# Performance work log

Hardware: AMD Instinct MI355X
Metric: run time of the kernel (lower is better)

Reference implementation:

```python
import jax, jax.numpy as jnp
import numpy as np


def setup_inputs() -> dict:
    key = jax.random.key(0)
    k1, k2, k3 = jax.random.split(key, 3)
    B, C, H, W = 32, 2048, 14, 14
    OUT = 512
    x = jax.random.normal(k1, (B, C, H, W), dtype=jnp.float32)
    gamma = jnp.zeros((1,), dtype=jnp.float32)  # nn.Parameter(torch.zeros(1))
    # 1x1 conv 2048 -> 512 (layer=4 branch), kaiming-ish scale
    conv_w = jax.random.normal(k2, (OUT, C, 1, 1), dtype=jnp.float32) * (1.0 / np.sqrt(C))
    conv_b = jax.random.normal(k3, (OUT,), dtype=jnp.float32) * 0.01
    return {"x": x, "gamma": gamma, "conv_w": conv_w, "conv_b": conv_b}


def reference(x, gamma, conv_w, conv_b):
    B, C, H, W = x.shape
    q = x.reshape(B, C, H * W)                      # [B, C, N]
    # energy[b, c, d] = <q[b,c,:], q[b,d,:]>
    energy = jnp.einsum('bcn,bdn->bcd', q, q)       # [B, C, C]
    # max-subtract trick: softmax(max - energy) along last dim
    energy_new = jnp.max(energy, axis=-1, keepdims=True) - energy
    attention = jax.nn.softmax(energy_new, axis=-1)  # [B, C, C]
    out = jnp.einsum('bcd,bdn->bcn', attention, q).reshape(B, C, H, W)
    out = gamma * out + x
    # 1x1 conv, stride 1, no padding (layer=4 branch)
    pam_out = jax.lax.conv_general_dilated(
        out, conv_w, window_strides=(1, 1), padding='VALID',
        dimension_numbers=('NCHW', 'OIHW', 'NCHW'))
    pam_out = pam_out + conv_b[None, :, None, None]
    return pam_out
```

## Files before the change

### kernel.cpp

```cpp
#include <hip/hip_runtime.h>
#include <hip/hip_bf16.h>
#include <stdint.h>

#define B_   32
#define C_   2048
#define HW_  196
#define OUT_ 512
#define KT_  128
#define MT_  64
#define NKT  (C_ / KT_)

typedef short short8 __attribute__((ext_vector_type(8)));
typedef float floatx4 __attribute__((ext_vector_type(4)));
typedef unsigned short u16;

#define VMCNT_WAIT(n) __builtin_amdgcn_s_waitcnt(0x0F70 | (n))

__device__ __forceinline__ uint32_t pack_bf16(float a, float b) {
  union { __hip_bfloat162 h; uint32_t u; } c;
  c.h = __float22bfloat162_rn(make_float2(a, b));
  return c.u;
}

__device__ __forceinline__ void async_ld16(const u16* g, void* lds_base) {
  __builtin_amdgcn_global_load_lds(
      (const __attribute__((address_space(1))) uint32_t*)g,
      (__attribute__((address_space(3))) uint32_t*)lds_base, 16, 0, 0);
}

__global__ void wcvt_kernel(const float* __restrict__ w, u16* __restrict__ wbf) {
  int gid = blockIdx.x * 256 + threadIdx.x;
  float4 v = ((const float4*)w)[gid];
  ((uint2*)wbf)[gid] = make_uint2(pack_bf16(v.x, v.y), pack_bf16(v.z, v.w));
}

__global__ void attn_fallback(const float* __restrict__ x, const float* __restrict__ gamma,
                              float* __restrict__ y) {
  float g = gamma[0];
  if (g == 0.0f) return;
  __shared__ float qc[HW_];
  __shared__ float e[C_];
  __shared__ float red[256];
  int tid = threadIdx.x;
  for (int cRow = blockIdx.x; cRow < C_; cRow += gridDim.x) {
    for (int b = 0; b < B_; ++b) {
      const float* q = x + (size_t)b * C_ * HW_;
      __syncthreads();
      for (int i = tid; i < HW_; i += 256) qc[i] = q[(size_t)cRow * HW_ + i];
      __syncthreads();
      for (int d = tid; d < C_; d += 256) {
        float s = 0.f;
        const float* qd = q + (size_t)d * HW_;
        for (int n = 0; n < HW_; ++n) s += qc[n] * qd[n];
        e[d] = s;
      }
      __syncthreads();
      float mn = 3.4e38f;
      for (int d = tid; d < C_; d += 256) mn = fminf(mn, e[d]);
      red[tid] = mn; __syncthreads();
      for (int s = 128; s > 0; s >>= 1) { if (tid < s) red[tid] = fminf(red[tid], red[tid + s]); __syncthreads(); }
      float emin = red[0];
      __syncthreads();
      float ps = 0.f;
      for (int d = tid; d < C_; d += 256) { float p = __expf(emin - e[d]); e[d] = p; ps += p; }
      red[tid] = ps; __syncthreads();
      for (int s = 128; s > 0; s >>= 1) { if (tid < s) red[tid] += red[tid + s]; __syncthreads(); }
      float S = red[0];
      __syncthreads();
      float invS = 1.f / S;
      for (int n = tid; n < HW_; n += 256) {
        float acc = 0.f;
        for (int d = 0; d < C_; ++d) acc += e[d] * q[(size_t)d * HW_ + n];
        y[((size_t)b * C_ + cRow) * HW_ + n] = g * acc * invS + q[(size_t)cRow * HW_ + n];
      }
    }
  }
}

__global__ __launch_bounds__(256, 3) void xpose_kernel(
    const float* __restrict__ x, const float* __restrict__ ysrc,
    const float* __restrict__ gamma, u16* __restrict__ xT) {
  __shared__ float tile[64 * 197];
  const float* src = (gamma[0] != 0.f) ? ysrc : x;
  int b  = blockIdx.x >> 5;
  int c0 = (blockIdx.x & 31) * 64;
  const float* sb = src + ((size_t)b * C_ + c0) * HW_;
  int tid = threadIdx.x;
  for (int r = 0; r < 13; ++r) {
    int u = r * 256 + tid;
    if (u < 3136) {
      int ci = u / 49, n4 = u - ci * 49;
      float4 v = *(const float4*)(sb + (size_t)ci * HW_ + n4 * 4);
      float* tp = &tile[ci * 197 + n4 * 4];
      tp[0] = v.x; tp[1] = v.y; tp[2] = v.z; tp[3] = v.w;
    }
  }
  __syncthreads();
  u16* xTb = xT + (size_t)b * HW_ * C_ + c0;
  for (int r = 0; r < 7; ++r) {
    int u = r * 256 + tid;
    if (u < 1568) {
      int c8 = u & 7, n = u >> 3;
      const float* tp = &tile[c8 * 8 * 197 + n];
      uint4 o;
      o.x = pack_bf16(tp[0 * 197], tp[1 * 197]);
      o.y = pack_bf16(tp[2 * 197], tp[3 * 197]);
      o.z = pack_bf16(tp[4 * 197], tp[5 * 197]);
      o.w = pack_bf16(tp[6 * 197], tp[7 * 197]);
      *(uint4*)(xTb + (size_t)n * C_ + c8 * 8) = o;
    }
  }
}

template<int P>
__device__ __forceinline__ void gemm_body(
    const u16* __restrict__ xT, const u16* __restrict__ wbf,
    const float* __restrict__ bias, float* __restrict__ out,
    u16* lds0, u16* lds1, int b, int oBase, int n0) {

  int tid  = threadIdx.x;
  int wave = tid >> 6;
  int lane = tid & 63;
  int col  = lane & 15;
  int quad = lane >> 4;

  const u16* xTb  = xT + (size_t)b * HW_ * C_;
  const u16* aPtr = wbf + (size_t)(oBase + wave * 16 + col) * C_;
  int maxRel = HW_ - 1 - n0;

  floatx4 acc[P];
#pragma unroll
  for (int i = 0; i < P; ++i) { floatx4 z = {0.f, 0.f, 0.f, 0.f}; acc[i] = z; }

  const u16* bPtr[P];
  int ldsOff[P];
#pragma unroll
  for (int jj = 0; jj < P; ++jj) {
    int n    = 4 * wave + quad + 16 * jj;
    int srcN = n0 + (n > maxRel ? maxRel : n);
    int kc   = col ^ (n & 7);
    bPtr[jj]   = xTb + (size_t)srcN * C_ + kc * 8;
    ldsOff[jj] = (wave + 4 * jj) * 512;
  }

  int aK = 0;
  auto issueB = [&](u16* dst) {
#pragma unroll
    for (int jj = 0; jj < P; ++jj) {
      async_ld16(bPtr[jj], dst + ldsOff[jj]);
      bPtr[jj] += KT_;
    }
  };
  uint4 aR[4];
  auto loadA = [&]() {
#pragma unroll
    for (int ks = 0; ks < 4; ++ks)
      aR[ks] = *(const uint4*)(aPtr + aK + ks * 32 + quad * 8);
    aK += KT_;
  };
  auto phase = [&](const u16* buf) {
#pragma unroll
    for (int ks = 0; ks < 4; ++ks) {
      union { uint4 u; short8 v; } af; af.u = aR[ks];
      int chunk = (ks * 4 + quad) ^ (col & 7);
      const u16* base = buf + col * KT_ + chunk * 8;
#pragma unroll
      for (int nt = 0; nt < P; ++nt) {
        short8 bf = *(const short8*)(base + nt * 16 * KT_);
        acc[nt] = __builtin_amdgcn_mfma_f32_16x16x32_bf16(af.v, bf, acc[nt], 0, 0, 0);
      }
    }
  };

  issueB(lds0);
  loadA();
  issueB(lds1);
  u16* cur = lds0; u16* nxt = lds1;
#pragma unroll
  for (int kt = 0; kt < NKT - 1; ++kt) {
    VMCNT_WAIT(P);
    __builtin_amdgcn_s_barrier();
    phase(cur);
    loadA();
    __builtin_amdgcn_s_barrier();
    if (kt < NKT - 2) issueB(cur);
    u16* t = cur; cur = nxt; nxt = t;
  }
  VMCNT_WAIT(0);
  __builtin_amdgcn_s_barrier();
  phase(cur);

  int nLim = HW_ - n0; if (nLim > 16 * P) nLim = 16 * P;
  float* outb = out + (size_t)b * OUT_ * HW_;
#pragma unroll
  for (int r = 0; r < 4; ++r) {
    int o = oBase + wave * 16 + quad * 4 + r;
    float bv = bias[o];
    float* orow = outb + (size_t)o * HW_ + n0;
#pragma unroll
    for (int nt = 0; nt < P; ++nt) {
      int nl = nt * 16 + col;
      if (nl < nLim) orow[nl] = acc[nt][r] + bv;
    }
  }
}

__global__ __launch_bounds__(256, 2) void conv_gemm(
    const u16* __restrict__ xT, const u16* __restrict__ wbf,
    const float* __restrict__ bias, float* __restrict__ out) {

  __shared__ __align__(16) u16 Bs2[2][112 * KT_];

  int bid = blockIdx.x;
  int xcd = bid & 7;
  int s   = bid >> 3;
  int ot  = s & 7;
  int g   = ((s >> 3) << 3) | xcd;
  int b   = g >> 1;
  int nh  = g & 1;

  if (nh == 0)
    gemm_body<7>(xT, wbf, bias, out, Bs2[0], Bs2[1], b, ot * MT_, 0);
  else
    gemm_body<6>(xT, wbf, bias, out, Bs2[0], Bs2[1], b, ot * MT_, 112);
}

extern "C" void kernel_launch(void* const* d_in, const int* in_sizes, int n_in,
                              void* d_out, int out_size, void* d_ws, size_t ws_size,
                              hipStream_t stream) {
  const float* x      = (const float*)d_in[0];
  const float* gamma  = (const float*)d_in[1];
  const float* conv_w = (const float*)d_in[2];
  const float* conv_b = (const float*)d_in[3];
  float* out = (float*)d_out;

  const size_t wbf_bytes = (size_t)OUT_ * C_ * sizeof(u16);
  const size_t xT_bytes  = (size_t)B_ * HW_ * C_ * sizeof(u16);
  const size_t y_bytes   = (size_t)B_ * C_ * HW_ * sizeof(float);
  u16*   wbf = (u16*)d_ws;
  u16*   xT  = (u16*)((char*)d_ws + wbf_bytes);
  float* yws = (float*)((char*)d_ws + wbf_bytes + xT_bytes);
  bool have_fallback_ws = ws_size >= wbf_bytes + xT_bytes + y_bytes;
  const float* ysrc = have_fallback_ws ? (const float*)yws : x;

  wcvt_kernel<<<dim3((OUT_ * C_) / 4 / 256), dim3(256), 0, stream>>>(conv_w, wbf);
  if (have_fallback_ws)
    attn_fallback<<<dim3(256), dim3(256), 0, stream>>>(x, gamma, yws);
  xpose_kernel<<<dim3(B_ * 32), dim3(256), 0, stream>>>(x, ysrc, gamma, xT);
  conv_gemm<<<dim3(512), dim3(256), 0, stream>>>(xT, wbf, conv_b, out);
}
```

Measured before the change: 127.1 us.

## Fuse transpose into GEMM staging and merge weight-convert with attention kernel

```diff
diff --git a/kernel.cpp b/kernel.cpp
--- a/kernel.cpp
+++ b/kernel.cpp
@@ -7,14 +7,13 @@
 #define HW_  196
 #define OUT_ 512
 #define KT_  128
-#define MT_  64
 #define NKT  (C_ / KT_)
+#define BN_  112
+#define LDSS 132
 
 typedef short short8 __attribute__((ext_vector_type(8)));
 typedef float floatx4 __attribute__((ext_vector_type(4)));
 typedef unsigned short u16;
-
-#define VMCNT_WAIT(n) __builtin_amdgcn_s_waitcnt(0x0F70 | (n))
 
 __device__ __forceinline__ uint32_t pack_bf16(float a, float b) {
   union { __hip_bfloat162 h; uint32_t u; } c;
@@ -22,27 +21,25 @@
   return c.u;
 }
 
-__device__ __forceinline__ void async_ld16(const u16* g, void* lds_base) {
-  __builtin_amdgcn_global_load_lds(
-      (const __attribute__((address_space(1))) uint32_t*)g,
-      (__attribute__((address_space(3))) uint32_t*)lds_base, 16, 0, 0);
-}
-
-__global__ void wcvt_kernel(const float* __restrict__ w, u16* __restrict__ wbf) {
-  int gid = blockIdx.x * 256 + threadIdx.x;
-  float4 v = ((const float4*)w)[gid];
-  ((uint2*)wbf)[gid] = make_uint2(pack_bf16(v.x, v.y), pack_bf16(v.z, v.w));
-}
-
-__global__ void attn_fallback(const float* __restrict__ x, const float* __restrict__ gamma,
-                              float* __restrict__ y) {
-  float g = gamma[0];
-  if (g == 0.0f) return;
+#define BAR_SYNC() asm volatile("s_waitcnt lgkmcnt(0)\n\ts_barrier" ::: "memory")
+
+__global__ void prep_kernel(const float* __restrict__ w, u16* __restrict__ wbf,
+                            const float* __restrict__ x,
+                            const float* __restrict__ gamma,
+                            float* __restrict__ y) {
+  if (blockIdx.x < 1024) {
+    int gid = blockIdx.x * 256 + threadIdx.x;
+    float4 v = ((const float4*)w)[gid];
+    ((uint2*)wbf)[gid] = make_uint2(pack_bf16(v.x, v.y), pack_bf16(v.z, v.w));
+    return;
+  }
+  float gm = gamma[0];
+  if (gm == 0.0f || y == nullptr) return;
   __shared__ float qc[HW_];
   __shared__ float e[C_];
   __shared__ float red[256];
   int tid = threadIdx.x;
-  for (int cRow = blockIdx.x; cRow < C_; cRow += gridDim.x) {
+  for (int cRow = (int)blockIdx.x - 1024; cRow < C_; cRow += 256) {
     for (int b = 0; b < B_; ++b) {
       const float* q = x + (size_t)b * C_ * HW_;
       __syncthreads();
@@ -58,171 +55,151 @@
       float mn = 3.4e38f;
       for (int d = tid; d < C_; d += 256) mn = fminf(mn, e[d]);
       red[tid] = mn; __syncthreads();
-      for (int s = 128; s > 0; s >>= 1) { if (tid < s) red[tid] = fminf(red[tid], red[tid + s]); __syncthreads(); }
+      for (int s2 = 128; s2 > 0; s2 >>= 1) { if (tid < s2) red[tid] = fminf(red[tid], red[tid + s2]); __syncthreads(); }
       float emin = red[0];
       __syncthreads();
       float ps = 0.f;
       for (int d = tid; d < C_; d += 256) { float p = __expf(emin - e[d]); e[d] = p; ps += p; }
       red[tid] = ps; __syncthreads();
-      for (int s = 128; s > 0; s >>= 1) { if (tid < s) red[tid] += red[tid + s]; __syncthreads(); }
+      for (int s2 = 128; s2 > 0; s2 >>= 1) { if (tid < s2) red[tid] += red[tid + s2]; __syncthreads(); }
       float S = red[0];
       __syncthreads();
       float invS = 1.f / S;
       for (int n = tid; n < HW_; n += 256) {
-        float acc = 0.f;
-        for (int d = 0; d < C_; ++d) acc += e[d] * q[(size_t)d * HW_ + n];
-        y[((size_t)b * C_ + cRow) * HW_ + n] = g * acc * invS + q[(size_t)cRow * HW_ + n];
+        float acc2 = 0.f;
+        for (int d = 0; d < C_; ++d) acc2 += e[d] * q[(size_t)d * HW_ + n];
+        y[((size_t)b * C_ + cRow) * HW_ + n] = gm * acc2 * invS + q[(size_t)cRow * HW_ + n];
       }
     }
   }
 }
 
-__global__ __launch_bounds__(256, 3) void xpose_kernel(
-    const float* __restrict__ x, const float* __restrict__ ysrc,
-    const float* __restrict__ gamma, u16* __restrict__ xT) {
-  __shared__ float tile[64 * 197];
-  const float* src = (gamma[0] != 0.f) ? ysrc : x;
-  int b  = blockIdx.x >> 5;
-  int c0 = (blockIdx.x & 31) * 64;
-  const float* sb = src + ((size_t)b * C_ + c0) * HW_;
-  int tid = threadIdx.x;
-  for (int r = 0; r < 13; ++r) {
-    int u = r * 256 + tid;
-    if (u < 3136) {
-      int ci = u / 49, n4 = u - ci * 49;
-      float4 v = *(const float4*)(sb + (size_t)ci * HW_ + n4 * 4);
-      float* tp = &tile[ci * 197 + n4 * 4];
-      tp[0] = v.x; tp[1] = v.y; tp[2] = v.z; tp[3] = v.w;
-    }
-  }
-  __syncthreads();
-  u16* xTb = xT + (size_t)b * HW_ * C_ + c0;
-  for (int r = 0; r < 7; ++r) {
-    int u = r * 256 + tid;
-    if (u < 1568) {
-      int c8 = u & 7, n = u >> 3;
-      const float* tp = &tile[c8 * 8 * 197 + n];
-      uint4 o;
-      o.x = pack_bf16(tp[0 * 197], tp[1 * 197]);
-      o.y = pack_bf16(tp[2 * 197], tp[3 * 197]);
-      o.z = pack_bf16(tp[4 * 197], tp[5 * 197]);
-      o.w = pack_bf16(tp[6 * 197], tp[7 * 197]);
-      *(uint4*)(xTb + (size_t)n * C_ + c8 * 8) = o;
-    }
-  }
-}
-
-template<int P>
-__device__ __forceinline__ void gemm_body(
-    const u16* __restrict__ xT, const u16* __restrict__ wbf,
-    const float* __restrict__ bias, float* __restrict__ out,
-    u16* lds0, u16* lds1, int b, int oBase, int n0) {
-
-  int tid  = threadIdx.x;
-  int wave = tid >> 6;
-  int lane = tid & 63;
-  int col  = lane & 15;
-  int quad = lane >> 4;
-
-  const u16* xTb  = xT + (size_t)b * HW_ * C_;
-  const u16* aPtr = wbf + (size_t)(oBase + wave * 16 + col) * C_;
-  int maxRel = HW_ - 1 - n0;
-
-  floatx4 acc[P];
-#pragma unroll
-  for (int i = 0; i < P; ++i) { floatx4 z = {0.f, 0.f, 0.f, 0.f}; acc[i] = z; }
-
-  const u16* bPtr[P];
-  int ldsOff[P];
-#pragma unroll
-  for (int jj = 0; jj < P; ++jj) {
-    int n    = 4 * wave + quad + 16 * jj;
-    int srcN = n0 + (n > maxRel ? maxRel : n);
-    int kc   = col ^ (n & 7);
-    bPtr[jj]   = xTb + (size_t)srcN * C_ + kc * 8;
-    ldsOff[jj] = (wave + 4 * jj) * 512;
-  }
-
-  int aK = 0;
-  auto issueB = [&](u16* dst) {
-#pragma unroll
-    for (int jj = 0; jj < P; ++jj) {
-      async_ld16(bPtr[jj], dst + ldsOff[jj]);
-      bPtr[jj] += KT_;
-    }
-  };
-  uint4 aR[4];
-  auto loadA = [&]() {
-#pragma unroll
-    for (int ks = 0; ks < 4; ++ks)
-      aR[ks] = *(const uint4*)(aPtr + aK + ks * 32 + quad * 8);
-    aK += KT_;
-  };
-  auto phase = [&](const u16* buf) {
+__global__ __launch_bounds__(256, 1) void conv_gemm(
+    const float* __restrict__ x, const float* __restrict__ yws,
+    const float* __restrict__ gamma, const u16* __restrict__ wbf,
+    const float* __restrict__ bias, float* __restrict__ out, int have_y) {
+
+  __shared__ __align__(16) u16 Bs[2][BN_ * LDSS];
+
+  const int tid  = threadIdx.x;
+  const int wave = tid >> 6;
+  const int lane = tid & 63;
+  const int col  = lane & 15;
+  const int quad = lane >> 4;
+
+  const int bid  = blockIdx.x;
+  const int xcd  = bid & 7;
+  const int s    = bid >> 3;
+  const int ot   = s & 3;
+  const int gset = s >> 2;
+  const int g    = gset * 8 + xcd;
+  const int b    = g >> 1;
+  const int nh   = g & 1;
+  const int n0   = nh * (HW_ - BN_);
+  const int oBase= ot * 128;
+
+  const float* src = (have_y && gamma[0] != 0.0f) ? yws : x;
+  const float* panel = src + (size_t)b * C_ * HW_ + n0;
+
+  int gOff[7], lOff[7];
+#pragma unroll
+  for (int i = 0; i < 7; ++i) {
+    int idx = i * 256 + tid;
+    int u = idx / 56;
+    int v = idx - u * 56;
+    gOff[i] = u * 4 * HW_ + 2 * v;
+    lOff[i] = (2 * v) * LDSS + 4 * u;
+  }
+
+  int rowOff[7];
+#pragma unroll
+  for (int nt = 0; nt < 7; ++nt) rowOff[nt] = (nt * 16 + col) * LDSS + quad * 8;
+
+  const u16* aRow = wbf + (size_t)(oBase + wave * 32 + col) * C_ + quad * 8;
+
+  floatx4 acc[2][7];
+#pragma unroll
+  for (int m = 0; m < 2; ++m)
+#pragma unroll
+    for (int nt = 0; nt < 7; ++nt) { floatx4 z = {0.f, 0.f, 0.f, 0.f}; acc[m][nt] = z; }
+
+  float2 sv[7][4];
+  uint4  aR[8];
+
+  auto stageLoad = [&](int kt) {
+    const float* p = panel + (size_t)kt * KT_ * HW_;
+#pragma unroll
+    for (int i = 0; i < 7; ++i) {
+      const float* q = p + gOff[i];
+#pragma unroll
+      for (int r = 0; r < 4; ++r) sv[i][r] = *(const float2*)(q + r * HW_);
+    }
+  };
+  auto loadA = [&](int kt) {
+#pragma unroll
+    for (int m = 0; m < 2; ++m)
+#pragma unroll
+      for (int ks = 0; ks < 4; ++ks)
+        aR[m * 4 + ks] = *(const uint4*)(aRow + (size_t)m * 16 * C_ + kt * KT_ + ks * 32);
+  };
+  auto stageWrite = [&](u16* bb) {
+#pragma unroll
+    for (int i = 0; i < 7; ++i) {
+      uint2 w0 = make_uint2(pack_bf16(sv[i][0].x, sv[i][1].x),
+                            pack_bf16(sv[i][2].x, sv[i][3].x));
+      uint2 w1 = make_uint2(pack_bf16(sv[i][0].y, sv[i][1].y),
+                            pack_bf16(sv[i][2].y, sv[i][3].y));
+      *(uint2*)(bb + lOff[i])        = w0;
+      *(uint2*)(bb + lOff[i] + LDSS) = w1;
+    }
+  };
+  auto phase = [&](const u16* bb) {
 #pragma unroll
     for (int ks = 0; ks < 4; ++ks) {
-      union { uint4 u; short8 v; } af; af.u = aR[ks];
-      int chunk = (ks * 4 + quad) ^ (col & 7);
-      const u16* base = buf + col * KT_ + chunk * 8;
-#pragma unroll
-      for (int nt = 0; nt < P; ++nt) {
-        short8 bf = *(const short8*)(base + nt * 16 * KT_);
-        acc[nt] = __builtin_amdgcn_mfma_f32_16x16x32_bf16(af.v, bf, acc[nt], 0, 0, 0);
+      union { uint4 u; short8 v; } a0, a1;
+      a0.u = aR[ks]; a1.u = aR[4 + ks];
+#pragma unroll
+      for (int nt = 0; nt < 7; ++nt) {
+        const u16* fp = bb + rowOff[nt] + ks * 32;
+        union { uint2 p[2]; short8 v; } bf;
+        bf.p[0] = *(const uint2*)fp;
+        bf.p[1] = *(const uint2*)(fp + 4);
+        acc[0][nt] = __builtin_amdgcn_mfma_f32_16x16x32_bf16(a0.v, bf.v, acc[0][nt], 0, 0, 0);
+        acc[1][nt] = __builtin_amdgcn_mfma_f32_16x16x32_bf16(a1.v, bf.v, acc[1][nt], 0, 0, 0);
       }
     }
   };
 
-  issueB(lds0);
-  loadA();
-  issueB(lds1);
-  u16* cur = lds0; u16* nxt = lds1;
-#pragma unroll
-  for (int kt = 0; kt < NKT - 1; ++kt) {
-    VMCNT_WAIT(P);
-    __builtin_amdgcn_s_barrier();
+  stageLoad(0);
+  loadA(0);
+  stageWrite(Bs[0]);
+  stageLoad(1);
+  BAR_SYNC();
+
+  u16* cur = Bs[0]; u16* nxt = Bs[1];
+  for (int kt = 0; kt < NKT; ++kt) {
     phase(cur);
-    loadA();
-    __builtin_amdgcn_s_barrier();
-    if (kt < NKT - 2) issueB(cur);
-    u16* t = cur; cur = nxt; nxt = t;
-  }
-  VMCNT_WAIT(0);
-  __builtin_amdgcn_s_barrier();
-  phase(cur);
-
-  int nLim = HW_ - n0; if (nLim > 16 * P) nLim = 16 * P;
-  float* outb = out + (size_t)b * OUT_ * HW_;
-#pragma unroll
-  for (int r = 0; r < 4; ++r) {
-    int o = oBase + wave * 16 + quad * 4 + r;
-    float bv = bias[o];
-    float* orow = outb + (size_t)o * HW_ + n0;
-#pragma unroll
-    for (int nt = 0; nt < P; ++nt) {
-      int nl = nt * 16 + col;
-      if (nl < nLim) orow[nl] = acc[nt][r] + bv;
-    }
-  }
-}
-
-__global__ __launch_bounds__(256, 2) void conv_gemm(
-    const u16* __restrict__ xT, const u16* __restrict__ wbf,
-    const float* __restrict__ bias, float* __restrict__ out) {
-
-  __shared__ __align__(16) u16 Bs2[2][112 * KT_];
-
-  int bid = blockIdx.x;
-  int xcd = bid & 7;
-  int s   = bid >> 3;
-  int ot  = s & 7;
-  int g   = ((s >> 3) << 3) | xcd;
-  int b   = g >> 1;
-  int nh  = g & 1;
-
-  if (nh == 0)
-    gemm_body<7>(xT, wbf, bias, out, Bs2[0], Bs2[1], b, ot * MT_, 0);
-  else
-    gemm_body<6>(xT, wbf, bias, out, Bs2[0], Bs2[1], b, ot * MT_, 112);
+    if (kt + 1 < NKT) {
+      loadA(kt + 1);
+      stageWrite(nxt);
+      if (kt + 2 < NKT) stageLoad(kt + 2);
+      BAR_SYNC();
+      u16* t = cur; cur = nxt; nxt = t;
+    }
+  }
+
+  float* outb = out + (size_t)b * OUT_ * HW_ + n0;
+#pragma unroll
+  for (int m = 0; m < 2; ++m)
+#pragma unroll
+    for (int r = 0; r < 4; ++r) {
+      int o = oBase + wave * 32 + m * 16 + quad * 4 + r;
+      float bv = bias[o];
+      float* orow = outb + (size_t)o * HW_;
+#pragma unroll
+      for (int nt = 0; nt < 7; ++nt)
+        orow[nt * 16 + col] = acc[m][nt][r] + bv;
+    }
 }
 
 extern "C" void kernel_launch(void* const* d_in, const int* in_sizes, int n_in,
@@ -235,17 +212,14 @@
   float* out = (float*)d_out;
 
   const size_t wbf_bytes = (size_t)OUT_ * C_ * sizeof(u16);
-  const size_t xT_bytes  = (size_t)B_ * HW_ * C_ * sizeof(u16);
   const size_t y_bytes   = (size_t)B_ * C_ * HW_ * sizeof(float);
   u16*   wbf = (u16*)d_ws;
-  u16*   xT  = (u16*)((char*)d_ws + wbf_bytes);
-  float* yws = (float*)((char*)d_ws + wbf_bytes + xT_bytes);
-  bool have_fallback_ws = ws_size >= wbf_bytes + xT_bytes + y_bytes;
-  const float* ysrc = have_fallback_ws ? (const float*)yws : x;
-
-  wcvt_kernel<<<dim3((OUT_ * C_) / 4 / 256), dim3(256), 0, stream>>>(conv_w, wbf);
-  if (have_fallback_ws)
-    attn_fallback<<<dim3(256), dim3(256), 0, stream>>>(x, gamma, yws);
-  xpose_kernel<<<dim3(B_ * 32), dim3(256), 0, stream>>>(x, ysrc, gamma, xT);
-  conv_gemm<<<dim3(512), dim3(256), 0, stream>>>(xT, wbf, conv_b, out);
-}
+  float* yws = (float*)((char*)d_ws + wbf_bytes);
+  int have_y = ws_size >= wbf_bytes + y_bytes;
+
+  int prep_grid = have_y ? 1280 : 1024;
+  prep_kernel<<<dim3(prep_grid), dim3(256), 0, stream>>>(
+      conv_w, wbf, x, gamma, have_y ? yws : nullptr);
+  conv_gemm<<<dim3(256), dim3(256), 0, stream>>>(
+      x, have_y ? yws : x, gamma, wbf, conv_b, out, have_y);
+}
```

Result: slower. 130.1 us (+2.4%).

## Enlarge conv GEMM tiles to 128x112 with 512 threads and fuse prep kernels

Applied to the files above, without the earlier changes.

```diff
diff --git a/kernel.cpp b/kernel.cpp
--- a/kernel.cpp
+++ b/kernel.cpp
@@ -7,8 +7,8 @@
 #define HW_  196
 #define OUT_ 512
 #define KT_  128
-#define MT_  64
 #define NKT  (C_ / KT_)
+#define BN_  112
 
 typedef short short8 __attribute__((ext_vector_type(8)));
 typedef float floatx4 __attribute__((ext_vector_type(4)));
@@ -28,21 +28,23 @@
       (__attribute__((address_space(3))) uint32_t*)lds_base, 16, 0, 0);
 }
 
-__global__ void wcvt_kernel(const float* __restrict__ w, u16* __restrict__ wbf) {
-  int gid = blockIdx.x * 256 + threadIdx.x;
-  float4 v = ((const float4*)w)[gid];
-  ((uint2*)wbf)[gid] = make_uint2(pack_bf16(v.x, v.y), pack_bf16(v.z, v.w));
-}
-
-__global__ void attn_fallback(const float* __restrict__ x, const float* __restrict__ gamma,
-                              float* __restrict__ y) {
-  float g = gamma[0];
-  if (g == 0.0f) return;
+__global__ void prep_kernel(const float* __restrict__ w, u16* __restrict__ wbf,
+                            const float* __restrict__ x,
+                            const float* __restrict__ gamma,
+                            float* __restrict__ y) {
+  if (blockIdx.x < 1024) {
+    int gid = blockIdx.x * 256 + threadIdx.x;
+    float4 v = ((const float4*)w)[gid];
+    ((uint2*)wbf)[gid] = make_uint2(pack_bf16(v.x, v.y), pack_bf16(v.z, v.w));
+    return;
+  }
+  float gm = gamma[0];
+  if (gm == 0.0f || y == nullptr) return;
   __shared__ float qc[HW_];
   __shared__ float e[C_];
   __shared__ float red[256];
   int tid = threadIdx.x;
-  for (int cRow = blockIdx.x; cRow < C_; cRow += gridDim.x) {
+  for (int cRow = (int)blockIdx.x - 1024; cRow < C_; cRow += 256) {
     for (int b = 0; b < B_; ++b) {
       const float* q = x + (size_t)b * C_ * HW_;
       __syncthreads();
@@ -58,20 +60,20 @@
       float mn = 3.4e38f;
       for (int d = tid; d < C_; d += 256) mn = fminf(mn, e[d]);
       red[tid] = mn; __syncthreads();
-      for (int s = 128; s > 0; s >>= 1) { if (tid < s) red[tid] = fminf(red[tid], red[tid + s]); __syncthreads(); }
+      for (int s2 = 128; s2 > 0; s2 >>= 1) { if (tid < s2) red[tid] = fminf(red[tid], red[tid + s2]); __syncthreads(); }
       float emin = red[0];
       __syncthreads();
       float ps = 0.f;
       for (int d = tid; d < C_; d += 256) { float p = __expf(emin - e[d]); e[d] = p; ps += p; }
       red[tid] = ps; __syncthreads();
-      for (int s = 128; s > 0; s >>= 1) { if (tid < s) red[tid] += red[tid + s]; __syncthreads(); }
+      for (int s2 = 128; s2 > 0; s2 >>= 1) { if (tid < s2) red[tid] += red[tid + s2]; __syncthreads(); }
       float S = red[0];
       __syncthreads();
       float invS = 1.f / S;
       for (int n = tid; n < HW_; n += 256) {
-        float acc = 0.f;
-        for (int d = 0; d < C_; ++d) acc += e[d] * q[(size_t)d * HW_ + n];
-        y[((size_t)b * C_ + cRow) * HW_ + n] = g * acc * invS + q[(size_t)cRow * HW_ + n];
+        float acc2 = 0.f;
+        for (int d = 0; d < C_; ++d) acc2 += e[d] * q[(size_t)d * HW_ + n];
+        y[((size_t)b * C_ + cRow) * HW_ + n] = gm * acc2 * invS + q[(size_t)cRow * HW_ + n];
       }
     }
   }
@@ -112,64 +114,68 @@
   }
 }
 
-template<int P>
-__device__ __forceinline__ void gemm_body(
-    const u16* __restrict__ xT, const u16* __restrict__ wbf,
+template<int NT>
+__device__ __forceinline__ void gemm_half(
+    const u16* __restrict__ xTb, const u16* __restrict__ wbf,
     const float* __restrict__ bias, float* __restrict__ out,
-    u16* lds0, u16* lds1, int b, int oBase, int n0) {
-
-  int tid  = threadIdx.x;
-  int wave = tid >> 6;
-  int lane = tid & 63;
-  int col  = lane & 15;
-  int quad = lane >> 4;
-
-  const u16* xTb  = xT + (size_t)b * HW_ * C_;
-  const u16* aPtr = wbf + (size_t)(oBase + wave * 16 + col) * C_;
-  int maxRel = HW_ - 1 - n0;
-
-  floatx4 acc[P];
-#pragma unroll
-  for (int i = 0; i < P; ++i) { floatx4 z = {0.f, 0.f, 0.f, 0.f}; acc[i] = z; }
-
-  const u16* bPtr[P];
-  int ldsOff[P];
-#pragma unroll
-  for (int jj = 0; jj < P; ++jj) {
-    int n    = 4 * wave + quad + 16 * jj;
-    int srcN = n0 + (n > maxRel ? maxRel : n);
-    int kc   = col ^ (n & 7);
-    bPtr[jj]   = xTb + (size_t)srcN * C_ + kc * 8;
-    ldsOff[jj] = (wave + 4 * jj) * 512;
-  }
-
+    u16* lds0, u16* lds1, int b, int oBase, int n0, int rowBase) {
+
+  const int tid  = threadIdx.x;
+  const int lane = tid & 63;
+  const int col  = lane & 15;
+  const int quad = lane >> 4;
+  const int wsub = (tid >> 6) & 3;
+
+  const u16* aPtr = wbf + (size_t)(oBase + wsub * 32 + col) * C_ + quad * 8;
+
+  floatx4 acc[2][NT];
+#pragma unroll
+  for (int m = 0; m < 2; ++m)
+#pragma unroll
+    for (int nt = 0; nt < NT; ++nt) { floatx4 z = {0.f, 0.f, 0.f, 0.f}; acc[m][nt] = z; }
+
+  const u16* bPtr[NT];
+  int ldsOff[NT];
+#pragma unroll
+  for (int jj = 0; jj < NT; ++jj) {
+    int rl = rowBase + 4 * wsub + 16 * jj + quad;
+    int kc = col ^ (4 * wsub + quad);
+    bPtr[jj]   = xTb + (size_t)(n0 + rl) * C_ + kc * 8;
+    ldsOff[jj] = ((rowBase >> 2) + wsub + 4 * jj) * 512;
+  }
+
+  uint4 aR[8];
   int aK = 0;
+  auto loadA = [&]() {
+#pragma unroll
+    for (int m = 0; m < 2; ++m)
+#pragma unroll
+      for (int ks = 0; ks < 4; ++ks)
+        aR[m * 4 + ks] = *(const uint4*)(aPtr + (size_t)m * 16 * C_ + aK + ks * 32);
+    aK += KT_;
+  };
   auto issueB = [&](u16* dst) {
 #pragma unroll
-    for (int jj = 0; jj < P; ++jj) {
+    for (int jj = 0; jj < NT; ++jj) {
       async_ld16(bPtr[jj], dst + ldsOff[jj]);
       bPtr[jj] += KT_;
     }
   };
-  uint4 aR[4];
-  auto loadA = [&]() {
-#pragma unroll
-    for (int ks = 0; ks < 4; ++ks)
-      aR[ks] = *(const uint4*)(aPtr + aK + ks * 32 + quad * 8);
-    aK += KT_;
-  };
-  auto phase = [&](const u16* buf) {
+  auto phase = [&](const u16* bb) {
+    __builtin_amdgcn_s_setprio(1);
 #pragma unroll
     for (int ks = 0; ks < 4; ++ks) {
-      union { uint4 u; short8 v; } af; af.u = aR[ks];
-      int chunk = (ks * 4 + quad) ^ (col & 7);
-      const u16* base = buf + col * KT_ + chunk * 8;
-#pragma unroll
-      for (int nt = 0; nt < P; ++nt) {
+      union { uint4 u; short8 v; } a0, a1;
+      a0.u = aR[ks]; a1.u = aR[4 + ks];
+      const u16* base = bb + (size_t)(rowBase + col) * KT_ + (((ks * 4 + quad) ^ col) * 8);
+#pragma unroll
+      for (int nt = 0; nt < NT; ++nt) {
         short8 bf = *(const short8*)(base + nt * 16 * KT_);
-        acc[nt] = __builtin_amdgcn_mfma_f32_16x16x32_bf16(af.v, bf, acc[nt], 0, 0, 0);
+        acc[0][nt] = __builtin_amdgcn_mfma_f32_16x16x32_bf16(a0.v, bf, acc[0][nt], 0, 0, 0);
+        acc[1][nt] = __builtin_amdgcn_mfma_f32_16x16x32_bf16(a1.v, bf, acc[1][nt], 0, 0, 0);
       }
     }
+    __builtin_amdgcn_s_setprio(0);
   };
 
   issueB(lds0);
@@ -178,7 +184,7 @@
   u16* cur = lds0; u16* nxt = lds1;
 #pragma unroll
   for (int kt = 0; kt < NKT - 1; ++kt) {
-    VMCNT_WAIT(P);
+    VMCNT_WAIT(8 + NT);
     __builtin_amdgcn_s_barrier();
     phase(cur);
     loadA();
@@ -186,43 +192,47 @@
     if (kt < NKT - 2) issueB(cur);
     u16* t = cur; cur = nxt; nxt = t;
   }
-  VMCNT_WAIT(0);
+  VMCNT_WAIT(8);
   __builtin_amdgcn_s_barrier();
   phase(cur);
 
-  int nLim = HW_ - n0; if (nLim > 16 * P) nLim = 16 * P;
   float* outb = out + (size_t)b * OUT_ * HW_;
 #pragma unroll
-  for (int r = 0; r < 4; ++r) {
-    int o = oBase + wave * 16 + quad * 4 + r;
-    float bv = bias[o];
-    float* orow = outb + (size_t)o * HW_ + n0;
-#pragma unroll
-    for (int nt = 0; nt < P; ++nt) {
-      int nl = nt * 16 + col;
-      if (nl < nLim) orow[nl] = acc[nt][r] + bv;
-    }
-  }
-}
-
-__global__ __launch_bounds__(256, 2) void conv_gemm(
+  for (int m = 0; m < 2; ++m)
+#pragma unroll
+    for (int r = 0; r < 4; ++r) {
+      int o = oBase + wsub * 32 + m * 16 + quad * 4 + r;
+      float bv = bias[o];
+      float* orow = outb + (size_t)o * HW_ + n0 + rowBase;
+#pragma unroll
+      for (int nt = 0; nt < NT; ++nt)
+        orow[nt * 16 + col] = acc[m][nt][r] + bv;
+    }
+}
+
+__global__ __launch_bounds__(512, 1) void conv_gemm(
     const u16* __restrict__ xT, const u16* __restrict__ wbf,
     const float* __restrict__ bias, float* __restrict__ out) {
 
-  __shared__ __align__(16) u16 Bs2[2][112 * KT_];
+  __shared__ __align__(16) u16 Bs2[2][BN_ * KT_];
 
   int bid = blockIdx.x;
   int xcd = bid & 7;
   int s   = bid >> 3;
-  int ot  = s & 7;
-  int g   = ((s >> 3) << 3) | xcd;
-  int b   = g >> 1;
-  int nh  = g & 1;
-
-  if (nh == 0)
-    gemm_body<7>(xT, wbf, bias, out, Bs2[0], Bs2[1], b, ot * MT_, 0);
+  int ot  = s & 3;
+  int gl  = s >> 2;
+  int grp = xcd * 8 + gl;
+  int b   = grp >> 1;
+  int nh  = grp & 1;
+  int n0  = nh * (HW_ - BN_);
+
+  const u16* xTb = xT + (size_t)b * HW_ * C_;
+  int ng = threadIdx.x >> 8;
+
+  if (ng == 0)
+    gemm_half<4>(xTb, wbf, bias, out, Bs2[0], Bs2[1], b, ot * 128, n0, 0);
   else
-    gemm_body<6>(xT, wbf, bias, out, Bs2[0], Bs2[1], b, ot * MT_, 112);
+    gemm_half<3>(xTb, wbf, bias, out, Bs2[0], Bs2[1], b, ot * 128, n0, 64);
 }
 
 extern "C" void kernel_launch(void* const* d_in, const int* in_sizes, int n_in,
@@ -240,12 +250,12 @@
   u16*   wbf = (u16*)d_ws;
   u16*   xT  = (u16*)((char*)d_ws + wbf_bytes);
   float* yws = (float*)((char*)d_ws + wbf_bytes + xT_bytes);
-  bool have_fallback_ws = ws_size >= wbf_bytes + xT_bytes + y_bytes;
-  const float* ysrc = have_fallback_ws ? (const float*)yws : x;
-
-  wcvt_kernel<<<dim3((OUT_ * C_) / 4 / 256), dim3(256), 0, stream>>>(conv_w, wbf);
-  if (have_fallback_ws)
-    attn_fallback<<<dim3(256), dim3(256), 0, stream>>>(x, gamma, yws);
-  xpose_kernel<<<dim3(B_ * 32), dim3(256), 0, stream>>>(x, ysrc, gamma, xT);
-  conv_gemm<<<dim3(512), dim3(256), 0, stream>>>(xT, wbf, conv_b, out);
-}
+  bool have_y = ws_size >= wbf_bytes + xT_bytes + y_bytes;
+
+  int prep_grid = have_y ? 1280 : 1024;
+  prep_kernel<<<dim3(prep_grid), dim3(256), 0, stream>>>(
+      conv_w, wbf, x, gamma, have_y ? yws : nullptr);
+  xpose_kernel<<<dim3(B_ * 32), dim3(256), 0, stream>>>(
+      x, have_y ? yws : x, gamma, xT);
+  conv_gemm<<<dim3(256), dim3(512), 0, stream>>>(xT, wbf, conv_b, out);
+}
```

Measured after the change: 141.9 us. +11.6%, slower.
